# Performance work log

Measured on AMD Instinct MI355X. Metric: run time of the kernel, lower is better.

Reference implementation:

```python
import jax, jax.numpy as jnp
import numpy as np

N = 100000  # nodes
EPS_BN = 1e-5
EPS_NORM = 1e-12


def sage_conv(x, edge_index, wl, bl, wr):
    # PyG SAGEConv (aggr='mean', normalize=True, project=False):
    # out = lin_l(mean_{j in N(i)} x_j) + lin_r(x_i); then L2-normalize rows.
    src, dst = edge_index[0], edge_index[1]
    msgs = x[src]                                            # [E, C] gather
    agg = jax.ops.segment_sum(msgs, dst, num_segments=N)     # [N, C]
    cnt = jax.ops.segment_sum(jnp.ones((edge_index.shape[1],), x.dtype), dst,
                              num_segments=N)                # [N]
    agg = agg / jnp.maximum(cnt, 1.0)[:, None]               # mean (0 for isolated)
    out = agg @ wl.T + bl + x @ wr.T                         # lin_l has bias, lin_r doesn't
    nrm = jnp.sqrt(jnp.sum(out * out, axis=-1, keepdims=True))
    return out / jnp.maximum(nrm, EPS_NORM)


def batch_norm(x, gamma, beta):
    # BatchNorm1d in training mode: batch stats, biased variance
    mean = jnp.mean(x, axis=0)
    var = jnp.mean((x - mean) ** 2, axis=0)
    return gamma * (x - mean) * jax.lax.rsqrt(var + EPS_BN) + beta


def setup_inputs() -> dict:
    key = jax.random.key(0)
    ks = jax.random.split(key, 9)
    C_in, C_h, C_out = 128, 128, 47
    E = 800000
    x = jax.random.normal(ks[0], (N, C_in), dtype=jnp.float32)
    edge_index = jax.random.randint(ks[1], (2, E), 0, N, dtype=jnp.int64)
    s = 0.1
    return {
        "x": x,
        "edge_index": edge_index,
        "w1l": jax.random.normal(ks[2], (C_h, C_in), dtype=jnp.float32) * s,
        "b1l": jnp.zeros((C_h,), dtype=jnp.float32),
        "w1r": jax.random.normal(ks[3], (C_h, C_in), dtype=jnp.float32) * s,
        "bn_gamma": jnp.ones((C_h,), dtype=jnp.float32),
        "bn_beta": jnp.zeros((C_h,), dtype=jnp.float32),
        "w2l": jax.random.normal(ks[4], (C_out, C_h), dtype=jnp.float32) * s,
        "b2l": jnp.zeros((C_out,), dtype=jnp.float32),
        "w2r": jax.random.normal(ks[5], (C_out, C_h), dtype=jnp.float32) * s,
    }


def reference(x, edge_index, w1l, b1l, w1r, bn_gamma, bn_beta, w2l, b2l, w2r):
    h = sage_conv(x, edge_index, w1l, b1l, w1r)   # [N, 128]
    h = batch_norm(h, bn_gamma, bn_beta)
    h = jax.nn.relu(h)
    # dropout p=0.0 -> identity
    out = sage_conv(h, edge_index, w2l, b2l, w2r)  # [N, 47]
    return out
```

## Files before the change

kernel.cpp:

```cpp
#include <hip/hip_runtime.h>
#include <cstdint>


typedef __attribute__((ext_vector_type(8))) short s8v;
typedef __attribute__((ext_vector_type(4))) short s4v;
typedef __attribute__((ext_vector_type(4))) float fx4;

#define CSR_CHUNK 8192
#define CSR_SH 8
#define CSR_NBPAD 512
#define CSR_BUFCAP 3072
#define PREP_XBLOCKS 1950

static __device__ __forceinline__ float bf2f(unsigned short h) {
    union { unsigned int u; float f; } c; c.u = (unsigned int)h << 16; return c.f;
}
static __device__ __forceinline__ unsigned short f2bf(float f) {
    union { float f; unsigned int u; } c; c.f = f;
    unsigned int u = c.u;
    return (unsigned short)((u + 0x7FFF + ((u >> 16) & 1)) >> 16);
}

__global__ __launch_bounds__(256) void k_prep(
        const float* __restrict__ x, const float* __restrict__ w1l,
        const float* __restrict__ w1r, const float* __restrict__ w2l,
        const float* __restrict__ w2r, const int* __restrict__ ei,
        unsigned short* __restrict__ xb, unsigned short* __restrict__ wB1,
        unsigned short* __restrict__ wB2p, float* __restrict__ stats,
        int* __restrict__ counts, int* __restrict__ bucketStart,
        int* __restrict__ gcur, int* __restrict__ done,
        int n, int nE, int nCh, int NB) {
    __shared__ int shm[1792];
    __shared__ int isLast;
    int t = threadIdx.x;
    if ((int)blockIdx.x < nCh) {
        int* hist = shm;
        int chunk = blockIdx.x;
        hist[t] = 0; hist[t + 256] = 0;
        __syncthreads();
        int e0 = chunk * CSR_CHUNK;
        int e1 = min(e0 + CSR_CHUNK, nE);
        for (int e = e0 + t; e < e1; e += 256)
            atomicAdd(&hist[ei[nE + e] >> CSR_SH], 1);
        __syncthreads();
        counts[chunk * CSR_NBPAD + t] = hist[t];
        counts[chunk * CSR_NBPAD + t + 256] = hist[t + 256];
        __threadfence();
        if (t == 0) isLast = (atomicAdd(done, 1) == nCh - 1);
        __syncthreads();
        if (!isLast) return;
        __threadfence();
        int* tot  = shm;
        int* tot2 = shm + 512;
        int* sh   = shm + 1024;
        int* bs   = shm + 1280;
        int tl = t & 127, g = t >> 7;
        int half = (nCh + 1) >> 1;
        int c0 = g * half, c1 = min(nCh, c0 + half);
        int4 s4 = {0, 0, 0, 0};
        for (int c = c0; c < c1; ++c) {
            int4 v = *(const int4*)(counts + (size_t)c * CSR_NBPAD + tl * 4);
            s4.x += v.x; s4.y += v.y; s4.z += v.z; s4.w += v.w;
        }
        __syncthreads();
        *(int4*)((g ? tot2 : tot) + tl * 4) = s4;
        __syncthreads();
        tot[t] += tot2[t];
        tot[t + 256] += tot2[t + 256];
        __syncthreads();
        int pairSum = tot[2 * t] + tot[2 * t + 1];
        sh[t] = pairSum;
        __syncthreads();
        for (int off = 1; off < 256; off <<= 1) {
            int add = (t >= off) ? sh[t - off] : 0;
            __syncthreads();
            sh[t] += add;
            __syncthreads();
        }
        int excl = sh[t] - pairSum;
        bs[2 * t] = excl;
        bs[2 * t + 1] = excl + tot[2 * t];
        __syncthreads();
        for (int b = t; b <= NB; b += 256) bucketStart[b] = bs[b];
        for (int b = t; b < CSR_NBPAD; b += 256) gcur[b] = bs[b];
        return;
    }
    int nx = n * 16;
    int total = nx + 32768 + 16384 + 2048;
    int stride = (gridDim.x - nCh) * 256;
    for (int idx0 = ((int)blockIdx.x - nCh) * 256 + t; idx0 < total; idx0 += stride) {
        int idx = idx0;
        if (idx < nx) {
            float4 a = ((const float4*)x)[idx * 2];
            float4 b = ((const float4*)x)[idx * 2 + 1];
            union { s8v v; unsigned short u[8]; } o;
            o.u[0] = f2bf(a.x); o.u[1] = f2bf(a.y); o.u[2] = f2bf(a.z); o.u[3] = f2bf(a.w);
            o.u[4] = f2bf(b.x); o.u[5] = f2bf(b.y); o.u[6] = f2bf(b.z); o.u[7] = f2bf(b.w);
            ((s8v*)xb)[idx] = o.v;
            continue;
        }
        idx -= nx;
        if (idx < 32768) {
            int j = idx >> 8, k = idx & 255;
            float v = (k < 128) ? w1l[j * 128 + k] : w1r[j * 128 + (k - 128)];
            wB1[idx] = f2bf(v);
            continue;
        }
        idx -= 32768;
        if (idx < 16384) {
            int j = idx >> 7, k = idx & 127;
            float v = 0.f;
            if (j < 47)      v = w2l[j * 128 + k];
            else if (j < 94) v = w2r[(j - 47) * 128 + k];
            wB2p[idx] = f2bf(v);
            continue;
        }
        idx -= 16384;
        if (idx < 2048) stats[idx] = 0.f;
    }
}

__global__ __launch_bounds__(256) void k_bfill(
        const int* __restrict__ ei, const int* __restrict__ counts,
        int* __restrict__ gcur, int* __restrict__ pairs, int nE) {
    __shared__ int cur[CSR_NBPAD];
    int t = threadIdx.x;
    #pragma unroll
    for (int i = 0; i < 2; ++i) {
        int b = t + i * 256;
        int h = counts[blockIdx.x * CSR_NBPAD + b];
        cur[b] = h ? atomicAdd(&gcur[b], h) : 0;
    }
    __syncthreads();
    int e0 = blockIdx.x * CSR_CHUNK;
    int e1 = min(e0 + CSR_CHUNK, nE);
    for (int e = e0 + t; e < e1; e += 256) {
        int s = ei[e];
        int d = ei[nE + e];
        int p = atomicAdd(&cur[d >> CSR_SH], 1);
        pairs[p] = (s << 8) | (d & 255);
    }
}

__global__ __launch_bounds__(256) void k_csr(
        const int* __restrict__ pairs, const int* __restrict__ bucketStart,
        int* __restrict__ deg, int* __restrict__ rowStart,
        int* __restrict__ srcIdx, int n) {
    __shared__ int cnt[256], scn[256], cur[256];
    __shared__ int buf[CSR_BUFCAP];
    int t = threadIdx.x;
    int bkt = blockIdx.x;
    int eBeg = bucketStart[bkt], eEnd = bucketStart[bkt + 1];
    int node0 = bkt << CSR_SH;
    cnt[t] = 0;
    __syncthreads();
    for (int e = eBeg + t; e < eEnd; e += 256)
        atomicAdd(&cnt[pairs[e] & 255], 1);
    __syncthreads();
    int myc = cnt[t];
    scn[t] = myc;
    __syncthreads();
    for (int off = 1; off < 256; off <<= 1) {
        int add = (t >= off) ? scn[t - off] : 0;
        __syncthreads();
        scn[t] += add;
        __syncthreads();
    }
    int excl = scn[t] - myc;
    cur[t] = excl;
    int node = node0 + t;
    if (node < n) { deg[node] = myc; rowStart[node] = eBeg + excl; }
    __syncthreads();
    for (int e = eBeg + t; e < eEnd; e += 256) {
        int pk = pairs[e];
        int p = atomicAdd(&cur[pk & 255], 1);
        int src = pk >> 8;
        if (p < CSR_BUFCAP) buf[p] = src;
        else srcIdx[eBeg + p] = src;
    }
    __syncthreads();
    int m = min(eEnd - eBeg, CSR_BUFCAP);
    for (int i = t; i < m; i += 256) srcIdx[eBeg + i] = buf[i];
}

__global__ __launch_bounds__(256) void k_gather1(
        const unsigned short* __restrict__ xb, const int* __restrict__ rowStart,
        const int* __restrict__ deg, const int* __restrict__ srcIdx,
        unsigned short* __restrict__ aggb, int n) {
    int t = threadIdx.x;
    int q = t & 15, grp = t >> 4;
    int node = blockIdx.x * 16 + grp;
    if (node >= n) return;
    int beg = rowStart[node];
    int d = deg[node];
    int end = beg + d;
    float a0[8] = {}, a1[8] = {}, a2[8] = {}, a3[8] = {};
    int e = beg;
    for (; e + 4 <= end; e += 4) {
        int s0 = srcIdx[e], s1v = srcIdx[e + 1], s2 = srcIdx[e + 2], s3 = srcIdx[e + 3];
        s8v v0 = *(const s8v*)(xb + (size_t)s0 * 128 + q * 8);
        s8v v1 = *(const s8v*)(xb + (size_t)s1v * 128 + q * 8);
        s8v v2 = *(const s8v*)(xb + (size_t)s2 * 128 + q * 8);
        s8v v3 = *(const s8v*)(xb + (size_t)s3 * 128 + q * 8);
        #pragma unroll
        for (int u = 0; u < 8; ++u) {
            a0[u] += bf2f((unsigned short)v0[u]);
            a1[u] += bf2f((unsigned short)v1[u]);
            a2[u] += bf2f((unsigned short)v2[u]);
            a3[u] += bf2f((unsigned short)v3[u]);
        }
    }
    for (; e < end; ++e) {
        s8v v0 = *(const s8v*)(xb + (size_t)srcIdx[e] * 128 + q * 8);
        #pragma unroll
        for (int u = 0; u < 8; ++u) a0[u] += bf2f((unsigned short)v0[u]);
    }
    float ic = 1.0f / fmaxf((float)d, 1.0f);
    union { s8v v; unsigned short u[8]; } o;
    #pragma unroll
    for (int u = 0; u < 8; ++u)
        o.u[u] = f2bf((a0[u] + a1[u] + a2[u] + a3[u]) * ic);
    *(s8v*)(aggb + (size_t)node * 128 + q * 8) = o.v;
}

#define GLL16(GSRC, LDST) \
    __builtin_amdgcn_global_load_lds( \
        (__attribute__((address_space(1))) void*)(void*)(GSRC), \
        (__attribute__((address_space(3))) void*)(LDST), 16, 0, 0)

__global__ __launch_bounds__(256, 4) void k_gemm1(
        const unsigned short* __restrict__ xb, const unsigned short* __restrict__ aggb,
        const unsigned short* __restrict__ wB1, const float* __restrict__ b1l,
        unsigned short* __restrict__ s1b, float* __restrict__ stats, int n) {
    __shared__ __align__(16) unsigned short xs[64 * 32];
    __shared__ __align__(16) unsigned short ws[128 * 32];
    __shared__ float norm2[128];
    __shared__ float invn[64];
    __shared__ float statS[256];
    __shared__ float statQ[256];
    int t = threadIdx.x;
    int w = t >> 6, L = t & 63;
    int q = L >> 4, lm = L & 15;
    int wr0 = (w >> 1) * 32;
    int wc0 = (w & 1) * 64;
    int r0 = blockIdx.x * 64;

    fx4 acc[2][4];
    fx4 z4 = {0.f, 0.f, 0.f, 0.f};
    #pragma unroll
    for (int r = 0; r < 2; ++r)
        #pragma unroll
        for (int c = 0; c < 4; ++c) acc[r][c] = z4;

    for (int kt = 0; kt < 8; ++kt) {
        const unsigned short* src = (kt < 4) ? aggb : xb;
        int kbase = (kt & 3) * 32;
        __syncthreads();
        {
            int row = t >> 2, p = t & 3;
            int sl = p ^ ((row >> 1) & 3);
            int gr = r0 + row; gr = gr < n ? gr : (n - 1);
            GLL16(src + (size_t)gr * 128 + kbase + sl * 8, &xs[t * 8]);
            #pragma unroll
            for (int it = 0; it < 2; ++it) {
                int i = t + it * 256;
                int wrow = i >> 2, wp = i & 3;
                int wsl = wp ^ ((wrow >> 1) & 3);
                GLL16(wB1 + (size_t)wrow * 256 + kt * 32 + wsl * 8, &ws[i * 8]);
            }
        }
        __syncthreads();
        s8v af[2], bfr[4];
        #pragma unroll
        for (int r = 0; r < 2; ++r) {
            int row = wr0 + r * 16 + lm;
            af[r] = *(const s8v*)&xs[row * 32 + ((q ^ ((row >> 1) & 3)) << 3)];
        }
        #pragma unroll
        for (int c = 0; c < 4; ++c) {
            int row = wc0 + c * 16 + lm;
            bfr[c] = *(const s8v*)&ws[row * 32 + ((q ^ ((row >> 1) & 3)) << 3)];
        }
        #pragma unroll
        for (int r = 0; r < 2; ++r)
            #pragma unroll
            for (int c = 0; c < 4; ++c)
                acc[r][c] = __builtin_amdgcn_mfma_f32_16x16x32_bf16(af[r], bfr[c], acc[r][c], 0, 0, 0);
    }

    float bj[4];
    #pragma unroll
    for (int c = 0; c < 4; ++c) bj[c] = b1l[wc0 + c * 16 + lm];
    #pragma unroll
    for (int r = 0; r < 2; ++r)
        #pragma unroll
        for (int c = 0; c < 4; ++c) acc[r][c] += bj[c];

    fx4 pr[2];
    #pragma unroll
    for (int r = 0; r < 2; ++r) {
        fx4 p = acc[r][0] * acc[r][0];
        #pragma unroll
        for (int c = 1; c < 4; ++c) p += acc[r][c] * acc[r][c];
        #pragma unroll
        for (int off = 1; off <= 8; off <<= 1)
            #pragma unroll
            for (int i2 = 0; i2 < 4; ++i2) p[i2] += __shfl_xor(p[i2], off, 64);
        pr[r] = p;
    }

    __syncthreads();
    if (lm == 0) {
        #pragma unroll
        for (int r = 0; r < 2; ++r)
            #pragma unroll
            for (int i = 0; i < 4; ++i)
                norm2[(wr0 + r * 16 + q * 4 + i) * 2 + (w & 1)] = pr[r][i];
    }
    __syncthreads();
    if (t < 64) {
        float s = norm2[t * 2] + norm2[t * 2 + 1];
        invn[t] = 1.0f / fmaxf(sqrtf(s), 1e-12f);
    }
    __syncthreads();

    float cS[4] = {}, cQ[4] = {};
    #pragma unroll
    for (int r = 0; r < 2; ++r) {
        int rowb = wr0 + r * 16 + q * 4;
        fx4 iv = *(const fx4*)&invn[rowb];
        #pragma unroll
        for (int c = 0; c < 4; ++c) {
            fx4 v = acc[r][c] * iv;
            int col = wc0 + c * 16 + lm;
            #pragma unroll
            for (int i = 0; i < 4; ++i) {
                int gr = r0 + rowb + i;
                if (gr < n) {
                    s1b[(size_t)gr * 128 + col] = f2bf(v[i]);
                    cS[c] += v[i];
                    cQ[c] += v[i] * v[i];
                }
            }
        }
    }
    #pragma unroll
    for (int off = 16; off <= 32; off <<= 1)
        #pragma unroll
        for (int c = 0; c < 4; ++c) {
            cS[c] += __shfl_xor(cS[c], off, 64);
            cQ[c] += __shfl_xor(cQ[c], off, 64);
        }
    if (q == 0) {
        #pragma unroll
        for (int c = 0; c < 4; ++c) {
            int col = wc0 + c * 16 + lm;
            statS[col * 2 + (w >> 1)] = cS[c];
            statQ[col * 2 + (w >> 1)] = cQ[c];
        }
    }
    __syncthreads();
    if (t < 128) {
        float* sp = stats + ((int)blockIdx.x & 7) * 256;
        atomicAdd(&sp[t],       statS[t * 2] + statS[t * 2 + 1]);
        atomicAdd(&sp[128 + t], statQ[t * 2] + statQ[t * 2 + 1]);
    }
}

__global__ __launch_bounds__(256, 4) void k_gemm2(
        const unsigned short* __restrict__ s1b, const unsigned short* __restrict__ wB2p,
        const float* __restrict__ stats, const float* __restrict__ gamma,
        const float* __restrict__ beta, const float* __restrict__ b2l,
        unsigned short* __restrict__ y2b, float* __restrict__ rbuf, int n) {
    __shared__ __align__(16) unsigned short xs[64 * 32];
    __shared__ __align__(16) unsigned short ws[128 * 32];
    __shared__ __align__(16) float abuf[128];
    __shared__ __align__(16) float bbuf[128];
    int t = threadIdx.x;
    int w = t >> 6, L = t & 63;
    int q = L >> 4, lm = L & 15;
    int wr0 = (w >> 1) * 32, wc0 = (w & 1) * 64;
    int r0 = blockIdx.x * 64;

    if (t < 128) {
        float s = 0.f, qv = 0.f;
        #pragma unroll
        for (int k = 0; k < 8; ++k) {
            s  += stats[k * 256 + t];
            qv += stats[k * 256 + 128 + t];
        }
        float fn = (float)n;
        float mean = s / fn;
        float var = qv / fn - mean * mean;
        float istd = rsqrtf(var + 1e-5f);
        float a = gamma[t] * istd;
        abuf[t] = a;
        bbuf[t] = beta[t] - mean * a;
    }
    __syncthreads();

    fx4 acc[2][4];
    fx4 z4 = {0.f, 0.f, 0.f, 0.f};
    #pragma unroll
    for (int r = 0; r < 2; ++r)
        #pragma unroll
        for (int c = 0; c < 4; ++c) acc[r][c] = z4;

    for (int kt = 0; kt < 4; ++kt) {
        int kbase = kt * 32;
        __syncthreads();
        {
            int row = t >> 2, p = t & 3;
            int sl = p ^ ((row >> 1) & 3);
            int gr = r0 + row; gr = gr < n ? gr : (n - 1);
            GLL16(s1b + (size_t)gr * 128 + kbase + sl * 8, &xs[t * 8]);
            #pragma unroll
            for (int it = 0; it < 2; ++it) {
                int i = t + it * 256;
                int wrow = i >> 2, wp = i & 3;
                int wsl = wp ^ ((wrow >> 1) & 3);
                GLL16(wB2p + (size_t)wrow * 128 + kbase + wsl * 8, &ws[i * 8]);
            }
        }
        __syncthreads();
        int kb = kbase + q * 8;
        fx4 a0 = *(const fx4*)&abuf[kb];
        fx4 a1 = *(const fx4*)&abuf[kb + 4];
        fx4 b0 = *(const fx4*)&bbuf[kb];
        fx4 b1 = *(const fx4*)&bbuf[kb + 4];
        s8v af[2], bfr[4];
        #pragma unroll
        for (int r = 0; r < 2; ++r) {
            int row = wr0 + r * 16 + lm;
            s8v sv = *(const s8v*)&xs[row * 32 + ((q ^ ((row >> 1) & 3)) << 3)];
            union { s8v v; unsigned short u[8]; } o;
            #pragma unroll
            for (int u = 0; u < 4; ++u) {
                float h0 = fmaxf(fmaf(a0[u], bf2f((unsigned short)sv[u]), b0[u]), 0.f);
                float h1 = fmaxf(fmaf(a1[u], bf2f((unsigned short)sv[u + 4]), b1[u]), 0.f);
                o.u[u]     = f2bf(h0);
                o.u[u + 4] = f2bf(h1);
            }
            af[r] = o.v;
        }
        #pragma unroll
        for (int c = 0; c < 4; ++c) {
            int row = wc0 + c * 16 + lm;
            bfr[c] = *(const s8v*)&ws[row * 32 + ((q ^ ((row >> 1) & 3)) << 3)];
        }
        #pragma unroll
        for (int r = 0; r < 2; ++r)
            #pragma unroll
            for (int c = 0; c < 4; ++c)
                acc[r][c] = __builtin_amdgcn_mfma_f32_16x16x32_bf16(af[r], bfr[c], acc[r][c], 0, 0, 0);
    }

    #pragma unroll
    for (int c = 0; c < 4; ++c) {
        int col = wc0 + c * 16 + lm;
        float bb = (col >= 47 && col < 94) ? b2l[col - 47] : 0.f;
        #pragma unroll
        for (int r = 0; r < 2; ++r) {
            int rowb = wr0 + r * 16 + q * 4;
            #pragma unroll
            for (int i = 0; i < 4; ++i) {
                int gr = r0 + rowb + i;
                if (gr >= n) continue;
                float v = acc[r][c][i];
                if (col < 47)      y2b[(size_t)gr * 64 + col] = f2bf(v);
                else if (col < 94) rbuf[(size_t)gr * 48 + (col - 47)] = v + bb;
            }
        }
    }
}

__global__ __launch_bounds__(256) void k_gather2_final(
        const unsigned short* __restrict__ y2b, const float* __restrict__ rbuf,
        const int* __restrict__ rowStart, const int* __restrict__ deg,
        const int* __restrict__ srcIdx, float* __restrict__ out, int n) {
    int t = threadIdx.x;
    int q = t & 15, grp = t >> 4;
    int node = blockIdx.x * 16 + grp;
    if (node >= n) return;
    int beg = rowStart[node];
    int d = deg[node];
    int end = beg + d;
    float acc[4] = {0.f, 0.f, 0.f, 0.f};
    int e = beg;
    for (; e + 8 <= end; e += 8) {
        int s0 = srcIdx[e],     s1v = srcIdx[e + 1];
        int s2 = srcIdx[e + 2], s3  = srcIdx[e + 3];
        int s4 = srcIdx[e + 4], s5  = srcIdx[e + 5];
        int s6 = srcIdx[e + 6], s7  = srcIdx[e + 7];
        s4v v0 = *(const s4v*)(y2b + (size_t)s0 * 64 + q * 4);
        s4v v1 = *(const s4v*)(y2b + (size_t)s1v * 64 + q * 4);
        s4v v2 = *(const s4v*)(y2b + (size_t)s2 * 64 + q * 4);
        s4v v3 = *(const s4v*)(y2b + (size_t)s3 * 64 + q * 4);
        s4v v4 = *(const s4v*)(y2b + (size_t)s4 * 64 + q * 4);
        s4v v5 = *(const s4v*)(y2b + (size_t)s5 * 64 + q * 4);
        s4v v6 = *(const s4v*)(y2b + (size_t)s6 * 64 + q * 4);
        s4v v7 = *(const s4v*)(y2b + (size_t)s7 * 64 + q * 4);
        #pragma unroll
        for (int u = 0; u < 4; ++u) {
            acc[u] += (bf2f((unsigned short)v0[u]) + bf2f((unsigned short)v1[u]))
                    + (bf2f((unsigned short)v2[u]) + bf2f((unsigned short)v3[u]))
                    + (bf2f((unsigned short)v4[u]) + bf2f((unsigned short)v5[u]))
                    + (bf2f((unsigned short)v6[u]) + bf2f((unsigned short)v7[u]));
        }
    }
    for (; e + 4 <= end; e += 4) {
        int s0 = srcIdx[e],     s1v = srcIdx[e + 1];
        int s2 = srcIdx[e + 2], s3  = srcIdx[e + 3];
        s4v v0 = *(const s4v*)(y2b + (size_t)s0 * 64 + q * 4);
        s4v v1 = *(const s4v*)(y2b + (size_t)s1v * 64 + q * 4);
        s4v v2 = *(const s4v*)(y2b + (size_t)s2 * 64 + q * 4);
        s4v v3 = *(const s4v*)(y2b + (size_t)s3 * 64 + q * 4);
        #pragma unroll
        for (int u = 0; u < 4; ++u)
            acc[u] += (bf2f((unsigned short)v0[u]) + bf2f((unsigned short)v1[u]))
                    + (bf2f((unsigned short)v2[u]) + bf2f((unsigned short)v3[u]));
    }
    for (; e < end; ++e) {
        s4v v0 = *(const s4v*)(y2b + (size_t)srcIdx[e] * 64 + q * 4);
        #pragma unroll
        for (int u = 0; u < 4; ++u) acc[u] += bf2f((unsigned short)v0[u]);
    }
    float ic = 1.0f / fmaxf((float)d, 1.0f);
    fx4 rb = *(const fx4*)(rbuf + (size_t)node * 48 + q * 4);
    float vi[4];
    float ss = 0.f;
    #pragma unroll
    for (int u = 0; u < 4; ++u) {
        int ch = q * 4 + u;
        float v = (ch < 47) ? (acc[u] * ic + rb[u]) : 0.f;
        vi[u] = v;
        ss += v * v;
    }
    #pragma unroll
    for (int off = 1; off <= 8; off <<= 1) ss += __shfl_xor(ss, off, 64);
    float inv = 1.0f / fmaxf(sqrtf(ss), 1e-12f);
    #pragma unroll
    for (int u = 0; u < 4; ++u) {
        int ch = q * 4 + u;
        if (ch < 47) out[(size_t)node * 47 + ch] = vi[u] * inv;
    }
}

extern "C" void kernel_launch(void* const* d_in, const int* in_sizes, int n_in,
                              void* d_out, int out_size, void* d_ws, size_t ws_size,
                              hipStream_t stream) {
    const float* x     = (const float*)d_in[0];
    const int*   ei    = (const int*)d_in[1];
    const float* w1l   = (const float*)d_in[2];
    const float* b1l   = (const float*)d_in[3];
    const float* w1r   = (const float*)d_in[4];
    const float* gamma = (const float*)d_in[5];
    const float* beta  = (const float*)d_in[6];
    const float* w2l   = (const float*)d_in[7];
    const float* b2l   = (const float*)d_in[8];
    const float* w2r   = (const float*)d_in[9];
    float* out = (float*)d_out;

    int n  = in_sizes[0] / 128;
    int nE = in_sizes[1] / 2;

    int NB  = (n + 255) >> 8;
    int nCh = (nE + CSR_CHUNK - 1) / CSR_CHUNK;

    int* deg       = (int*)d_ws;
    float* stats   = (float*)(deg + n);
    int* rowStart  = (int*)(stats + 2048);
    int* meta      = rowStart + n;
    int* srcIdx    = meta + n;
    unsigned short* xb   = (unsigned short*)(srcIdx + nE);
    unsigned short* aggb = xb + (size_t)n * 128;
    unsigned short* s1b  = aggb + (size_t)n * 128;
    unsigned short* wB1  = s1b + (size_t)n * 128;
    unsigned short* wB2p = wB1 + 32768;
    int* counts      = meta;
    int* bucketStart = meta + 60000;
    int* gcur        = meta + 61000;
    int* done        = meta + 61600;
    int* pairs       = (int*)s1b;
    unsigned short* y2b = xb;
    float* rbuf = (float*)(y2b + (size_t)n * 64);

    hipMemsetAsync(done, 0, sizeof(int), stream);
    k_prep<<<nCh + PREP_XBLOCKS, 256, 0, stream>>>(
        x, w1l, w1r, w2l, w2r, ei, xb, wB1, wB2p, stats, counts,
        bucketStart, gcur, done, n, nE, nCh, NB);
    k_bfill<<<nCh, 256, 0, stream>>>(ei, counts, gcur, pairs, nE);
    k_csr<<<NB, 256, 0, stream>>>(pairs, bucketStart, deg, rowStart, srcIdx, n);
    k_gather1<<<(n + 15) / 16, 256, 0, stream>>>(xb, rowStart, deg, srcIdx, aggb, n);
    k_gemm1<<<(n + 63) / 64, 256, 0, stream>>>(xb, aggb, wB1, b1l, s1b, stats, n);
    k_gemm2<<<(n + 63) / 64, 256, 0, stream>>>(
        s1b, wB2p, stats, gamma, beta, b2l, y2b, rbuf, n);
    k_gather2_final<<<(n + 15) / 16, 256, 0, stream>>>(y2b, rbuf, rowStart, deg, srcIdx, out, n);
}
```

Measured before the change: 261.3 us.

## Replace last-block histogram reduction with global atomics and a separate scan kernel

The per-chunk bucket histograms are no longer stored to a counts array and reduced by a last-arriving block. Each chunk block now atomically adds its histogram into a global total, and a new single-block kernel does the prefix scan to produce bucket starts and cursors. The fill kernel recomputes its chunk's histogram locally instead of reading the stored counts, which trades an extra pass over destination indices for removing the serial tail reduction and the fence/done-counter logic. It also adds one more kernel launch.

```diff
diff --git a/kernel.cpp b/kernel.cpp
--- a/kernel.cpp
+++ b/kernel.cpp
@@ -27,14 +27,10 @@
         const float* __restrict__ w2r, const int* __restrict__ ei,
         unsigned short* __restrict__ xb, unsigned short* __restrict__ wB1,
         unsigned short* __restrict__ wB2p, float* __restrict__ stats,
-        int* __restrict__ counts, int* __restrict__ bucketStart,
-        int* __restrict__ gcur, int* __restrict__ done,
-        int n, int nE, int nCh, int NB) {
-    __shared__ int shm[1792];
-    __shared__ int isLast;
+        int* __restrict__ tot, int n, int nE, int nCh) {
+    __shared__ int hist[CSR_NBPAD];
     int t = threadIdx.x;
     if ((int)blockIdx.x < nCh) {
-        int* hist = shm;
         int chunk = blockIdx.x;
         hist[t] = 0; hist[t + 256] = 0;
         __syncthreads();
@@ -43,46 +39,8 @@
         for (int e = e0 + t; e < e1; e += 256)
             atomicAdd(&hist[ei[nE + e] >> CSR_SH], 1);
         __syncthreads();
-        counts[chunk * CSR_NBPAD + t] = hist[t];
-        counts[chunk * CSR_NBPAD + t + 256] = hist[t + 256];
-        __threadfence();
-        if (t == 0) isLast = (atomicAdd(done, 1) == nCh - 1);
-        __syncthreads();
-        if (!isLast) return;
-        __threadfence();
-        int* tot  = shm;
-        int* tot2 = shm + 512;
-        int* sh   = shm + 1024;
-        int* bs   = shm + 1280;
-        int tl = t & 127, g = t >> 7;
-        int half = (nCh + 1) >> 1;
-        int c0 = g * half, c1 = min(nCh, c0 + half);
-        int4 s4 = {0, 0, 0, 0};
-        for (int c = c0; c < c1; ++c) {
-            int4 v = *(const int4*)(counts + (size_t)c * CSR_NBPAD + tl * 4);
-            s4.x += v.x; s4.y += v.y; s4.z += v.z; s4.w += v.w;
-        }
-        __syncthreads();
-        *(int4*)((g ? tot2 : tot) + tl * 4) = s4;
-        __syncthreads();
-        tot[t] += tot2[t];
-        tot[t + 256] += tot2[t + 256];
-        __syncthreads();
-        int pairSum = tot[2 * t] + tot[2 * t + 1];
-        sh[t] = pairSum;
-        __syncthreads();
-        for (int off = 1; off < 256; off <<= 1) {
-            int add = (t >= off) ? sh[t - off] : 0;
-            __syncthreads();
-            sh[t] += add;
-            __syncthreads();
-        }
-        int excl = sh[t] - pairSum;
-        bs[2 * t] = excl;
-        bs[2 * t + 1] = excl + tot[2 * t];
-        __syncthreads();
-        for (int b = t; b <= NB; b += 256) bucketStart[b] = bs[b];
-        for (int b = t; b < CSR_NBPAD; b += 256) gcur[b] = bs[b];
+        if (hist[t])       atomicAdd(&tot[t],       hist[t]);
+        if (hist[t + 256]) atomicAdd(&tot[t + 256], hist[t + 256]);
         return;
     }
     int nx = n * 16;
@@ -120,20 +78,51 @@
     }
 }
 
+__global__ __launch_bounds__(256) void k_bmeta(
+        const int* __restrict__ tot, int* __restrict__ bucketStart,
+        int* __restrict__ gcur, int NB) {
+    __shared__ int tl[CSR_NBPAD], sh[256], bs[CSR_NBPAD];
+    int t = threadIdx.x;
+    tl[t] = tot[t];
+    tl[t + 256] = tot[t + 256];
+    __syncthreads();
+    int pairSum = tl[2 * t] + tl[2 * t + 1];
+    sh[t] = pairSum;
+    __syncthreads();
+    for (int off = 1; off < 256; off <<= 1) {
+        int add = (t >= off) ? sh[t - off] : 0;
+        __syncthreads();
+        sh[t] += add;
+        __syncthreads();
+    }
+    int excl = sh[t] - pairSum;
+    bs[2 * t] = excl;
+    bs[2 * t + 1] = excl + tl[2 * t];
+    __syncthreads();
+    for (int b = t; b <= NB; b += 256) bucketStart[b] = bs[b];
+    for (int b = t; b < CSR_NBPAD; b += 256) gcur[b] = bs[b];
+}
+
 __global__ __launch_bounds__(256) void k_bfill(
-        const int* __restrict__ ei, const int* __restrict__ counts,
-        int* __restrict__ gcur, int* __restrict__ pairs, int nE) {
+        const int* __restrict__ ei, int* __restrict__ gcur,
+        int* __restrict__ pairs, int nE) {
+    __shared__ int hist[CSR_NBPAD];
     __shared__ int cur[CSR_NBPAD];
     int t = threadIdx.x;
+    hist[t] = 0; hist[t + 256] = 0;
+    __syncthreads();
+    int e0 = blockIdx.x * CSR_CHUNK;
+    int e1 = min(e0 + CSR_CHUNK, nE);
+    for (int e = e0 + t; e < e1; e += 256)
+        atomicAdd(&hist[ei[nE + e] >> CSR_SH], 1);
+    __syncthreads();
     #pragma unroll
     for (int i = 0; i < 2; ++i) {
         int b = t + i * 256;
-        int h = counts[blockIdx.x * CSR_NBPAD + b];
+        int h = hist[b];
         cur[b] = h ? atomicAdd(&gcur[b], h) : 0;
     }
     __syncthreads();
-    int e0 = blockIdx.x * CSR_CHUNK;
-    int e1 = min(e0 + CSR_CHUNK, nE);
     for (int e = e0 + t; e < e1; e += 256) {
         int s = ei[e];
         int d = ei[nE + e];
@@ -577,19 +566,18 @@
     unsigned short* s1b  = aggb + (size_t)n * 128;
     unsigned short* wB1  = s1b + (size_t)n * 128;
     unsigned short* wB2p = wB1 + 32768;
-    int* counts      = meta;
     int* bucketStart = meta + 60000;
     int* gcur        = meta + 61000;
-    int* done        = meta + 61600;
+    int* tot         = meta + 61600;
     int* pairs       = (int*)s1b;
     unsigned short* y2b = xb;
     float* rbuf = (float*)(y2b + (size_t)n * 64);
 
-    hipMemsetAsync(done, 0, sizeof(int), stream);
+    hipMemsetAsync(tot, 0, CSR_NBPAD * sizeof(int), stream);
     k_prep<<<nCh + PREP_XBLOCKS, 256, 0, stream>>>(
-        x, w1l, w1r, w2l, w2r, ei, xb, wB1, wB2p, stats, counts,
-        bucketStart, gcur, done, n, nE, nCh, NB);
-    k_bfill<<<nCh, 256, 0, stream>>>(ei, counts, gcur, pairs, nE);
+        x, w1l, w1r, w2l, w2r, ei, xb, wB1, wB2p, stats, tot, n, nE, nCh);
+    k_bmeta<<<1, 256, 0, stream>>>(tot, bucketStart, gcur, NB);
+    k_bfill<<<nCh, 256, 0, stream>>>(ei, gcur, pairs, nE);
     k_csr<<<NB, 256, 0, stream>>>(pairs, bucketStart, deg, rowStart, srcIdx, n);
     k_gather1<<<(n + 15) / 16, 256, 0, stream>>>(xb, rowStart, deg, srcIdx, aggb, n);
     k_gemm1<<<(n + 63) / 64, 256, 0, stream>>>(xb, aggb, wB1, b1l, s1b, stats, n);
```

Result: faster. 250.6 us (-4.1%).
